# Optimization experiments

Hardware: AMD Instinct MI355X
Metric: run time of the kernel (lower is better)

## Reference

```python
import jax, jax.numpy as jnp
import numpy as np

B, C, H, W = 4, 512, 48, 48
DQ = C // 8  # inter_rate = 8
N = H * W
EPS = 1e-5


def _local_mask(radius):
    r = np.arange(N) // W
    c = np.arange(N) % W
    d = np.maximum(np.abs(r[:, None] - r[None, :]), np.abs(c[:, None] - c[None, :]))
    return jnp.asarray(d <= radius)


def setup_inputs() -> dict:
    key = jax.random.key(0)
    ks = jax.random.split(key, 12)
    def nrm(k, shape, scale=0.04):
        return jax.random.normal(k, shape, dtype=jnp.float32) * scale
    zc = jnp.zeros((C,), jnp.float32)
    oc = jnp.ones((C,), jnp.float32)
    return {
        "x": jax.random.normal(ks[0], (B, C, H, W), dtype=jnp.float32),
        "Wq": nrm(ks[1], (DQ, C)), "bq": jnp.zeros((DQ,), jnp.float32),
        "Wk": nrm(ks[2], (DQ, C)), "bk": jnp.zeros((DQ,), jnp.float32),
        "Wv": nrm(ks[3], (C, C)), "bv": zc,
        "conv1_w": nrm(ks[4], (C, C, 3, 3)),
        "bn1_w": oc, "bn1_b": zc, "bn1_m": zc, "bn1_v": oc,
        "conv2_w": nrm(ks[5], (C, C, 3, 3)),
        "bn2_w": oc, "bn2_b": zc, "bn2_m": zc, "bn2_v": oc,
        "sig1_w": nrm(ks[6], (C, C)), "sig1_b": zc,
        "sig2_w": nrm(ks[7], (C, C)), "sig2_b": zc,
        "gamma": jnp.full((1,), 0.5, jnp.float32),
        "gamma1": jnp.full((1,), 0.3, jnp.float32),
        "gamma2": jnp.full((1,), 0.2, jnp.float32),
        "mask1": _local_mask(6),
        "mask2": _local_mask(12),
    }


def _masked_softmax(e, mask):
    # exp(e)*mask / sum(exp(e)*mask) == softmax with -inf outside mask
    e = e - jnp.max(e, axis=-1, keepdims=True)
    w = jnp.exp(e) * mask.astype(e.dtype)
    return w / jnp.sum(w, axis=-1, keepdims=True)


def _conv1x1(t, w, b):
    return jnp.einsum('bchw,dc->bdhw', t, w) + b[None, :, None, None]


def _conv3x3_bn_relu(t, w, g, beta, mu, var):
    y = jax.lax.conv_general_dilated(t, w, (1, 1), 'SAME',
                                     dimension_numbers=('NCHW', 'OIHW', 'NCHW'))
    scale = (g / jnp.sqrt(var + EPS))[None, :, None, None]
    y = (y - mu[None, :, None, None]) * scale + beta[None, :, None, None]
    return jax.nn.relu(y)


def _forward(x, Wq, bq, Wk, bk, Wv, bv, conv1_w, bn1_w, bn1_b, bn1_m, bn1_v,
             conv2_w, bn2_w, bn2_b, bn2_m, bn2_v, sig1_w, sig1_b, sig2_w, sig2_b,
             gamma, gamma1, gamma2, mask1, mask2):
    b, c, h, w = x.shape
    n = h * w
    q = _conv1x1(x, Wq, bq).reshape(b, -1, n)   # [B, d, N]
    k = _conv1x1(x, Wk, bk).reshape(b, -1, n)   # [B, d, N]
    energy = jnp.einsum('bdn,bdm->bnm', q, k)   # [B, N, N] (query rows)
    a0 = jax.nn.softmax(energy, axis=-1)
    a1 = _masked_softmax(energy, mask1)
    a2 = _masked_softmax(energy, mask2)
    v = _conv1x1(x, Wv, bv).reshape(b, c, n)
    # torch: bmm(value, attention.permute(0,2,1)) -> out[b,c,m] = sum_n v[b,c,n]*a[m,n]
    out0 = jnp.einsum('bcn,bmn->bcm', v, a0).reshape(b, c, h, w)
    out0 = gamma * out0 + x
    out0 = _conv3x3_bn_relu(out0, conv1_w, bn1_w, bn1_b, bn1_m, bn1_v)
    s1 = (jax.nn.sigmoid(_conv1x1(out0, sig1_w, sig1_b)) * out0).reshape(b, c, n)
    out1 = jnp.einsum('bcn,bmn->bcm', s1, a1).reshape(b, c, h, w)
    out1 = gamma1 * out1 + out0
    out1 = _conv3x3_bn_relu(out1, conv2_w, bn2_w, bn2_b, bn2_m, bn2_v)
    s2 = (jax.nn.sigmoid(_conv1x1(out1, sig2_w, sig2_b)) * out1).reshape(b, c, n)
    out2 = jnp.einsum('bcn,bmn->bcm', s2, a2).reshape(b, c, h, w)
    return gamma2 * out2 + out1


def reference(x, Wq, bq, Wk, bk, Wv, bv, conv1_w, bn1_w, bn1_b, bn1_m, bn1_v,
              conv2_w, bn2_w, bn2_b, bn2_m, bn2_v, sig1_w, sig1_b, sig2_w, sig2_b,
              gamma, gamma1, gamma2, mask1, mask2):
    return _forward(x, Wq, bq, Wk, bk, Wv, bv, conv1_w, bn1_w, bn1_b, bn1_m, bn1_v,
                    conv2_w, bn2_w, bn2_b, bn2_m, bn2_v, sig1_w, sig1_b, sig2_w, sig2_b,
                    gamma, gamma1, gamma2, mask1, mask2)
```

## Files before the change

kernel.cpp:

```cpp
#include <hip/hip_runtime.h>
#include <math.h>

#define BB 4
#define CC 512
#define HH 48
#define WW 48
#define NN 2304
#define DDQ 64
#define LDSP 72
#define PW 50
#define PROWS 2500

typedef __attribute__((ext_vector_type(4))) float f32x4;
typedef __attribute__((ext_vector_type(8))) _Float16 half8;
typedef __attribute__((ext_vector_type(4))) _Float16 half4;

__device__ __forceinline__ int imax(int a, int b) { return a > b ? a : b; }
__device__ __forceinline__ int imin(int a, int b) { return a < b ? a : b; }
__device__ __forceinline__ int prow(int m) {
    int h = m / WW, w = m - h * WW;
    return (h + 1) * PW + (w + 1);
}

typedef __attribute__((address_space(1))) unsigned int g_u32;
typedef __attribute__((address_space(3))) unsigned int l_u32;
__device__ __forceinline__ void gl16(const _Float16* g, _Float16* l) {
    __builtin_amdgcn_global_load_lds((g_u32*)g, (l_u32*)l, 16, 0, 0);
}

#define BWAVE_IDX()                                  \
    int tid = threadIdx.x;                           \
    int wave = tid >> 6, lane = tid & 63;            \
    int wm = (wave >> 1) * 64, wn = (wave & 1) * 32; \
    int x = lane & 15, qq = lane >> 4;

__device__ __forceinline__ half8 fragld(const _Float16* T, int r, int c) {
    int kb = c ^ (r & 7);
    return *(const half8*)(T + r * 64 + kb * 8);
}

__device__ __forceinline__ void btile(const _Float16* As, const _Float16* Bs,
                                      f32x4 acc[4][2], int wm, int wn, int x, int qq) {
#pragma unroll
    for (int ks = 0; ks < 2; ++ks) {
        int c = ks * 4 + qq;
        half8 a0 = fragld(As, wm + x, c);
        half8 a1 = fragld(As, wm + 16 + x, c);
        half8 a2 = fragld(As, wm + 32 + x, c);
        half8 a3 = fragld(As, wm + 48 + x, c);
        half8 b0 = fragld(Bs, wn + x, c);
        half8 b1 = fragld(Bs, wn + 16 + x, c);
        acc[0][0] = __builtin_amdgcn_mfma_f32_16x16x32_f16(a0, b0, acc[0][0], 0, 0, 0);
        acc[0][1] = __builtin_amdgcn_mfma_f32_16x16x32_f16(a0, b1, acc[0][1], 0, 0, 0);
        acc[1][0] = __builtin_amdgcn_mfma_f32_16x16x32_f16(a1, b0, acc[1][0], 0, 0, 0);
        acc[1][1] = __builtin_amdgcn_mfma_f32_16x16x32_f16(a1, b1, acc[1][1], 0, 0, 0);
        acc[2][0] = __builtin_amdgcn_mfma_f32_16x16x32_f16(a2, b0, acc[2][0], 0, 0, 0);
        acc[2][1] = __builtin_amdgcn_mfma_f32_16x16x32_f16(a2, b1, acc[2][1], 0, 0, 0);
        acc[3][0] = __builtin_amdgcn_mfma_f32_16x16x32_f16(a3, b0, acc[3][0], 0, 0, 0);
        acc[3][1] = __builtin_amdgcn_mfma_f32_16x16x32_f16(a3, b1, acc[3][1], 0, 0, 0);
    }
}

#define BACC_INIT()                                         \
    f32x4 zf = {0.f, 0.f, 0.f, 0.f};                        \
    f32x4 acc[4][2];                                        \
    _Pragma("unroll") for (int i_ = 0; i_ < 4; ++i_) {      \
        acc[i_][0] = zf; acc[i_][1] = zf; }

#define SLOT_A(i) int sb = (wave * 4 + (i)) * 64; int s = sb + lane; \
                  int r = s >> 3, kb = s & 7; int koff = ((kb ^ (r & 7)) << 3);
#define SLOT_B(i) int sb = (wave * 2 + (i)) * 64; int s = sb + lane; \
                  int r = s >> 3, kb = s & 7; int koff = ((kb ^ (r & 7)) << 3);

__device__ __forceinline__ void stage_rows(_Float16* dst, const _Float16* __restrict__ src,
                                           int ld, int row0, int k0, int tid) {
#pragma unroll
    for (int i = 0; i < 2; ++i) {
        int s = tid * 2 + i;
        int r = s >> 3, off = (s & 7) << 3;
        *(half8*)(dst + r * LDSP + off) =
            *(const half8*)(src + (size_t)(row0 + r) * ld + k0 + off);
    }
}
__device__ __forceinline__ void mfma_tile(const _Float16* As, const _Float16* Bs,
                                          f32x4 acc[2][2], int wm, int wn, int x, int qq) {
#pragma unroll
    for (int ks = 0; ks < 2; ++ks) {
        int kof = ks * 32 + qq * 8;
        half8 a0 = *(const half8*)(As + (wm + x) * LDSP + kof);
        half8 a1 = *(const half8*)(As + (wm + 16 + x) * LDSP + kof);
        half8 b0 = *(const half8*)(Bs + (wn + x) * LDSP + kof);
        half8 b1 = *(const half8*)(Bs + (wn + 16 + x) * LDSP + kof);
        acc[0][0] = __builtin_amdgcn_mfma_f32_16x16x32_f16(a0, b0, acc[0][0], 0, 0, 0);
        acc[0][1] = __builtin_amdgcn_mfma_f32_16x16x32_f16(a0, b1, acc[0][1], 0, 0, 0);
        acc[1][0] = __builtin_amdgcn_mfma_f32_16x16x32_f16(a1, b0, acc[1][0], 0, 0, 0);
        acc[1][1] = __builtin_amdgcn_mfma_f32_16x16x32_f16(a1, b1, acc[1][1], 0, 0, 0);
    }
}
#define WAVE_IDX()                             \
    int tid = threadIdx.x;                     \
    int wave = tid >> 6, lane = tid & 63;      \
    int wm = (wave >> 1) * 32, wn = (wave & 1) * 32; \
    int x = lane & 15, qq = lane >> 4;
#define ACC_INIT()                             \
    f32x4 zf = {0.f, 0.f, 0.f, 0.f};           \
    f32x4 acc[2][2];                           \
    acc[0][0] = zf; acc[0][1] = zf; acc[1][0] = zf; acc[1][1] = zf;

__global__ __launch_bounds__(256) void k_f32_to_f16(const float* __restrict__ src,
                                                    _Float16* __restrict__ dst, int n) {
    for (int i = blockIdx.x * 256 + threadIdx.x; i < n; i += gridDim.x * 256)
        dst[i] = (_Float16)src[i];
}

__global__ __launch_bounds__(256) void k_repack_conv(const float* __restrict__ w,
                                                     _Float16* __restrict__ dst) {
    int i = blockIdx.x * 256 + threadIdx.x;
    if (i >= 9 * CC * CC) return;
    int r = i / (CC * CC);
    int rem = i - r * CC * CC;
    int co = rem / CC, ci = rem - (rem / CC) * CC;
    dst[i] = (_Float16)w[((size_t)co * CC + ci) * 9 + r];
}

__global__ __launch_bounds__(256) void k_transpose_x(const float* __restrict__ x,
                                                     _Float16* __restrict__ xT) {
    __shared__ float tile[32][33];
    int b = blockIdx.z;
    int c0 = blockIdx.y * 32, n0 = blockIdx.x * 32;
    int tx = threadIdx.x & 31, ty = threadIdx.x >> 5;
    const float* xb = x + (size_t)b * CC * NN;
#pragma unroll
    for (int rr = 0; rr < 32; rr += 8)
        tile[ty + rr][tx] = xb[(size_t)(c0 + ty + rr) * NN + n0 + tx];
    __syncthreads();
    _Float16* xTb = xT + (size_t)b * NN * CC;
#pragma unroll
    for (int rr = 0; rr < 32; rr += 8)
        xTb[(size_t)(n0 + ty + rr) * CC + c0 + tx] = (_Float16)tile[tx][ty + rr];
}

__global__ __launch_bounds__(256) void k_qkproj(const _Float16* __restrict__ Wq,
                                                const _Float16* __restrict__ Wk,
                                                const float* __restrict__ bq,
                                                const float* __restrict__ bk,
                                                const _Float16* __restrict__ xT,
                                                _Float16* __restrict__ qT,
                                                _Float16* __restrict__ kT) {
    __shared__ _Float16 As[64 * LDSP];
    __shared__ _Float16 Bs[64 * LDSP];
    WAVE_IDX();
    int j0 = blockIdx.x * 64, b = blockIdx.z;
    const _Float16* Wp = blockIdx.y ? Wk : Wq;
    const float* bias = blockIdx.y ? bk : bq;
    _Float16* outT = blockIdx.y ? kT : qT;
    const _Float16* xTb = xT + (size_t)b * NN * CC;
    ACC_INIT();
    for (int kc = 0; kc < CC; kc += 64) {
        stage_rows(As, Wp, CC, 0, kc, tid);
        stage_rows(Bs, xTb, CC, j0, kc, tid);
        __syncthreads();
        mfma_tile(As, Bs, acc, wm, wn, x, qq);
        __syncthreads();
    }
#pragma unroll
    for (int ms = 0; ms < 2; ++ms) {
        int R0 = wm + ms * 16 + qq * 4;
#pragma unroll
        for (int ns = 0; ns < 2; ++ns) {
            int Ccol = j0 + wn + ns * 16 + x;
            half4 t;
            t.x = (_Float16)(acc[ms][ns][0] + bias[R0 + 0]);
            t.y = (_Float16)(acc[ms][ns][1] + bias[R0 + 1]);
            t.z = (_Float16)(acc[ms][ns][2] + bias[R0 + 2]);
            t.w = (_Float16)(acc[ms][ns][3] + bias[R0 + 3]);
            *(half4*)(outT + ((size_t)b * NN + Ccol) * DDQ + R0) = t;
        }
    }
}

template <int EPI, int PAD>
__global__ __launch_bounds__(256) void k_cgemm(const _Float16* __restrict__ W,
                                               const float* __restrict__ bias,
                                               const _Float16* __restrict__ Bsrc,
                                               const float* __restrict__ gate,
                                               _Float16* __restrict__ out) {
    __shared__ _Float16 As[128 * 64];
    __shared__ _Float16 Bs[64 * 64];
    BWAVE_IDX();
    int j0 = blockIdx.x * 64, i0 = blockIdx.y * 128, b = blockIdx.z;
    const _Float16* Bb = Bsrc + (size_t)b * (PAD ? (size_t)PROWS * CC : (size_t)NN * CC);

    const _Float16* aSrc[4]; int aOf[4];
#pragma unroll
    for (int i = 0; i < 4; ++i) {
        SLOT_A(i);
        aSrc[i] = W + (size_t)(i0 + r) * CC + koff;
        aOf[i] = sb * 8;
    }
    const _Float16* bSrc[2]; int bOf[2];
#pragma unroll
    for (int i = 0; i < 2; ++i) {
        SLOT_B(i);
        int row = PAD ? prow(j0 + r) : (j0 + r);
        bSrc[i] = Bb + (size_t)row * CC + koff;
        bOf[i] = sb * 8;
    }
    BACC_INIT();
    for (int kc = 0; kc < CC; kc += 64) {
        __syncthreads();
#pragma unroll
        for (int i = 0; i < 4; ++i) gl16(aSrc[i] + kc, As + aOf[i]);
#pragma unroll
        for (int i = 0; i < 2; ++i) gl16(bSrc[i] + kc, Bs + bOf[i]);
        __syncthreads();
        btile(As, Bs, acc, wm, wn, x, qq);
    }
#pragma unroll
    for (int mt = 0; mt < 4; ++mt) {
        int R0 = i0 + wm + mt * 16 + qq * 4;
#pragma unroll
        for (int nt = 0; nt < 2; ++nt) {
            int Ccol = j0 + wn + nt * 16 + x;
#pragma unroll
            for (int e = 0; e < 4; ++e) {
                float v = acc[mt][nt][e] + bias[R0 + e];
                size_t idx = ((size_t)b * CC + R0 + e) * NN + Ccol;
                if (EPI == 1) v = gate[idx] / (1.f + __expf(-v));
                out[idx] = (_Float16)v;
            }
        }
    }
}

__global__ __launch_bounds__(256) void k_energy(const _Float16* __restrict__ qT,
                                                const _Float16* __restrict__ kT,
                                                float* __restrict__ E, int rad) {
    __shared__ _Float16 As[64 * LDSP];
    __shared__ _Float16 Bs[64 * LDSP];
    WAVE_IDX();
    int j0 = blockIdx.x * 64, i0 = blockIdx.y * 64, b = blockIdx.z;
    if (rad > 0) {
        int hlo = i0 / WW, hhi = (i0 + 63) / WW;
        int h2lo = imax(0, hlo - rad), h2hi = imin(HH - 1, hhi + rad);
        int nlo = (h2lo * WW) & ~63;
        int nhi = imin(NN, ((h2hi + 1) * WW + 63) & ~63);
        if (j0 + 64 <= nlo || j0 >= nhi) return;
    }
    ACC_INIT();
    stage_rows(As, qT + (size_t)b * NN * DDQ, DDQ, i0, 0, tid);
    stage_rows(Bs, kT + (size_t)b * NN * DDQ, DDQ, j0, 0, tid);
    __syncthreads();
    mfma_tile(As, Bs, acc, wm, wn, x, qq);
#pragma unroll
    for (int ms = 0; ms < 2; ++ms) {
        int R0 = i0 + wm + ms * 16 + qq * 4;
#pragma unroll
        for (int ns = 0; ns < 2; ++ns) {
            int Ccol = j0 + wn + ns * 16 + x;
#pragma unroll
            for (int e = 0; e < 4; ++e)
                E[((size_t)b * NN + R0 + e) * NN + Ccol] = acc[ms][ns][e];
        }
    }
}

__global__ __launch_bounds__(256) void k_softmax(float* __restrict__ E, int rad) {
    __shared__ float red[256];
    int tid = threadIdx.x;
    int m = blockIdx.x, b = blockIdx.y;
    float* e = E + ((size_t)b * NN + m) * NN;
    _Float16* a = (_Float16*)e;
    int own_lo = 0, own_hi = NN, nlo = 0, nhi = NN;
    int mcol = m % WW;
    if (rad > 0) {
        int hm = m / WW;
        int oh_lo = imax(0, hm - rad), oh_hi = imin(HH - 1, hm + rad);
        own_lo = oh_lo * WW; own_hi = (oh_hi + 1) * WW;
        int i0 = m & ~63;
        int hlo = i0 / WW, hhi = (i0 + 63) / WW;
        int h2lo = imax(0, hlo - rad), h2hi = imin(HH - 1, hhi + rad);
        nlo = (h2lo * WW) & ~63;
        nhi = imin(NN, ((h2hi + 1) * WW + 63) & ~63);
    }
    int v0 = own_lo >> 2, v1 = own_hi >> 2;

    float mx = -1e30f;
    for (int n4 = v0 + tid; n4 < v1; n4 += 256) {
        float4 v = *(const float4*)(e + n4 * 4);
        mx = fmaxf(fmaxf(fmaxf(mx, v.x), v.y), fmaxf(v.z, v.w));
    }
    red[tid] = mx; __syncthreads();
    for (int s = 128; s > 0; s >>= 1) {
        if (tid < s) red[tid] = fmaxf(red[tid], red[tid + s]);
        __syncthreads();
    }
    mx = red[0]; __syncthreads();

    f32x4 wloc[3];
    float ls = 0.f;
#pragma unroll
    for (int ii = 0; ii < 3; ++ii) {
        int n4 = v0 + tid + ii * 256;
        if (n4 < v1) {
            float4 v = *(const float4*)(e + n4 * 4);
            f32x4 w;
            w[0] = __expf(v.x - mx); w[1] = __expf(v.y - mx);
            w[2] = __expf(v.z - mx); w[3] = __expf(v.w - mx);
            if (rad > 0) {
                int cb = (n4 * 4) % WW;
#pragma unroll
                for (int j = 0; j < 4; ++j) {
                    int dc = mcol - (cb + j); if (dc < 0) dc = -dc;
                    if (dc > rad) w[j] = 0.f;
                }
            }
            wloc[ii] = w;
            ls += w[0] + w[1] + w[2] + w[3];
        }
    }
    red[tid] = ls; __syncthreads();
    for (int s = 128; s > 0; s >>= 1) {
        if (tid < s) red[tid] += red[tid + s];
        __syncthreads();
    }
    float inv = 1.f / red[0];
#pragma unroll
    for (int ii = 0; ii < 3; ++ii) {
        int n4 = v0 + tid + ii * 256;
        if (n4 < v1) {
            half4 h;
            h.x = (_Float16)(wloc[ii][0] * inv);
            h.y = (_Float16)(wloc[ii][1] * inv);
            h.z = (_Float16)(wloc[ii][2] * inv);
            h.w = (_Float16)(wloc[ii][3] * inv);
            *(half4*)(a + n4 * 4) = h;
        }
    }
    for (int n = nlo + tid; n < own_lo; n += 256) a[n] = (_Float16)0.f;
    for (int n = own_hi + tid; n < nhi; n += 256) a[n] = (_Float16)0.f;
}

__global__ __launch_bounds__(256) void k_attn(const _Float16* __restrict__ A,
                                              const _Float16* __restrict__ attn,
                                              const float* __restrict__ res,
                                              const float* __restrict__ gamma,
                                              float* __restrict__ outF,
                                              _Float16* __restrict__ outT, int rad) {
    __shared__ _Float16 As[128 * 64];
    __shared__ _Float16 Bs[64 * 64];
    BWAVE_IDX();
    int j0 = blockIdx.x * 64, i0 = blockIdx.y * 128, b = blockIdx.z;
    int klo = 0, khi = NN;
    if (rad > 0) {
        int hlo = j0 / WW, hhi = (j0 + 63) / WW;
        int h2lo = imax(0, hlo - rad), h2hi = imin(HH - 1, hhi + rad);
        klo = (h2lo * WW) & ~63;
        khi = imin(NN, ((h2hi + 1) * WW + 63) & ~63);
    }
    const _Float16* Ab = A + (size_t)b * CC * NN;
    const _Float16* Tb = attn + (size_t)b * NN * (2 * NN);

    const _Float16* aSrc[4]; int aOf[4];
#pragma unroll
    for (int i = 0; i < 4; ++i) {
        SLOT_A(i);
        aSrc[i] = Ab + (size_t)(i0 + r) * NN + koff;
        aOf[i] = sb * 8;
    }
    const _Float16* bSrc[2]; int bOf[2];
#pragma unroll
    for (int i = 0; i < 2; ++i) {
        SLOT_B(i);
        bSrc[i] = Tb + (size_t)(j0 + r) * (2 * NN) + koff;
        bOf[i] = sb * 8;
    }
    BACC_INIT();
    for (int kc = klo; kc < khi; kc += 64) {
        __syncthreads();
#pragma unroll
        for (int i = 0; i < 4; ++i) gl16(aSrc[i] + kc, As + aOf[i]);
#pragma unroll
        for (int i = 0; i < 2; ++i) gl16(bSrc[i] + kc, Bs + bOf[i]);
        __syncthreads();
        btile(As, Bs, acc, wm, wn, x, qq);
    }
    float g = gamma[0];
#pragma unroll
    for (int mt = 0; mt < 4; ++mt) {
        int R0 = i0 + wm + mt * 16 + qq * 4;
#pragma unroll
        for (int nt = 0; nt < 2; ++nt) {
            int Ccol = j0 + wn + nt * 16 + x;
            float v[4];
#pragma unroll
            for (int e = 0; e < 4; ++e)
                v[e] = g * acc[mt][nt][e] + res[((size_t)b * CC + R0 + e) * NN + Ccol];
            if (outT) {
                half4 t;
                t.x = (_Float16)v[0]; t.y = (_Float16)v[1];
                t.z = (_Float16)v[2]; t.w = (_Float16)v[3];
                *(half4*)(outT + ((size_t)b * PROWS + prow(Ccol)) * CC + R0) = t;
            }
            if (outF) {
#pragma unroll
                for (int e = 0; e < 4; ++e)
                    outF[((size_t)b * CC + R0 + e) * NN + Ccol] = v[e];
            }
        }
    }
}

__global__ __launch_bounds__(256) void k_conv3(const _Float16* __restrict__ Arep,
                                               const _Float16* __restrict__ Tpad,
                                               const float* __restrict__ bng,
                                               const float* __restrict__ bnb,
                                               const float* __restrict__ bnm,
                                               const float* __restrict__ bnv,
                                               float* __restrict__ outF,
                                               _Float16* __restrict__ outT) {
    __shared__ _Float16 As[128 * 64];
    __shared__ _Float16 Bs[64 * 64];
    BWAVE_IDX();
    int j0 = blockIdx.x * 64, i0 = blockIdx.y * 128, b = blockIdx.z;
    const _Float16* Tb = Tpad + (size_t)b * PROWS * CC;

    size_t aRow[4]; int aOf[4];
#pragma unroll
    for (int i = 0; i < 4; ++i) {
        SLOT_A(i);
        aRow[i] = (size_t)(i0 + r) * CC + koff;
        aOf[i] = sb * 8;
    }
    int bPr[2], bKoff[2], bOf[2];
#pragma unroll
    for (int i = 0; i < 2; ++i) {
        SLOT_B(i);
        bPr[i] = prow(j0 + r);
        bKoff[i] = koff;
        bOf[i] = sb * 8;
    }
    BACC_INIT();
#pragma unroll
    for (int rt = 0; rt < 9; ++rt) {
        int dh = rt / 3 - 1, dw = rt - (rt / 3) * 3 - 1;
        int shift = dh * PW + dw;
        const _Float16* Ar = Arep + (size_t)rt * CC * CC;
        for (int ci0 = 0; ci0 < CC; ci0 += 64) {
            __syncthreads();
#pragma unroll
            for (int i = 0; i < 4; ++i) gl16(Ar + aRow[i] + ci0, As + aOf[i]);
#pragma unroll
            for (int i = 0; i < 2; ++i)
                gl16(Tb + (size_t)(bPr[i] + shift) * CC + ci0 + bKoff[i], Bs + bOf[i]);
            __syncthreads();
            btile(As, Bs, acc, wm, wn, x, qq);
        }
    }
#pragma unroll
    for (int mt = 0; mt < 4; ++mt) {
        int R0 = i0 + wm + mt * 16 + qq * 4;
        float sc[4], sh[4];
#pragma unroll
        for (int e = 0; e < 4; ++e) {
            sc[e] = bng[R0 + e] * rsqrtf(bnv[R0 + e] + 1e-5f);
            sh[e] = bnb[R0 + e] - bnm[R0 + e] * sc[e];
        }
#pragma unroll
        for (int nt = 0; nt < 2; ++nt) {
            int Ccol = j0 + wn + nt * 16 + x;
            float v[4];
#pragma unroll
            for (int e = 0; e < 4; ++e) {
                float t = acc[mt][nt][e] * sc[e] + sh[e];
                v[e] = t > 0.f ? t : 0.f;
                outF[((size_t)b * CC + R0 + e) * NN + Ccol] = v[e];
            }
            half4 t4;
            t4.x = (_Float16)v[0]; t4.y = (_Float16)v[1];
            t4.z = (_Float16)v[2]; t4.w = (_Float16)v[3];
            *(half4*)(outT + ((size_t)b * PROWS + prow(Ccol)) * CC + R0) = t4;
        }
    }
}

extern "C" void kernel_launch(void* const* d_in, const int* in_sizes, int n_in,
                              void* d_out, int out_size, void* d_ws, size_t ws_size,
                              hipStream_t stream) {
    const float* xin  = (const float*)d_in[0];
    const float* Wq   = (const float*)d_in[1];
    const float* bq   = (const float*)d_in[2];
    const float* Wk   = (const float*)d_in[3];
    const float* bk   = (const float*)d_in[4];
    const float* Wv   = (const float*)d_in[5];
    const float* bv   = (const float*)d_in[6];
    const float* c1w  = (const float*)d_in[7];
    const float* bn1w = (const float*)d_in[8];
    const float* bn1b = (const float*)d_in[9];
    const float* bn1m = (const float*)d_in[10];
    const float* bn1v = (const float*)d_in[11];
    const float* c2w  = (const float*)d_in[12];
    const float* bn2w = (const float*)d_in[13];
    const float* bn2b = (const float*)d_in[14];
    const float* bn2m = (const float*)d_in[15];
    const float* bn2v = (const float*)d_in[16];
    const float* s1w  = (const float*)d_in[17];
    const float* s1b  = (const float*)d_in[18];
    const float* s2w  = (const float*)d_in[19];
    const float* s2b  = (const float*)d_in[20];
    const float* gamma  = (const float*)d_in[21];
    const float* gamma1 = (const float*)d_in[22];
    const float* gamma2 = (const float*)d_in[23];

    float* out = (float*)d_out;

    char* p = (char*)d_ws;
    float*    E     = (float*)p;    p += (size_t)BB * NN * NN * 4;
    _Float16* xT    = (_Float16*)p; p += (size_t)BB * NN * CC * 2;
    _Float16* qT    = (_Float16*)p; p += (size_t)BB * NN * DDQ * 2;
    _Float16* kT    = (_Float16*)p; p += (size_t)BB * NN * DDQ * 2;
    _Float16* vsB   = (_Float16*)p; p += (size_t)BB * CC * NN * 2;
    _Float16* TattnP= (_Float16*)p; p += (size_t)BB * PROWS * CC * 2;
    _Float16* TconvP= (_Float16*)p; p += (size_t)BB * PROWS * CC * 2;
    float*    rR    = (float*)p;    p += (size_t)BB * CC * NN * 4;
    _Float16* wq_h  = (_Float16*)p; p += (size_t)DDQ * CC * 2;
    _Float16* wk_h  = (_Float16*)p; p += (size_t)DDQ * CC * 2;
    _Float16* wv_h  = (_Float16*)p; p += (size_t)CC * CC * 2;
    _Float16* s1_h  = (_Float16*)p; p += (size_t)CC * CC * 2;
    _Float16* s2_h  = (_Float16*)p; p += (size_t)CC * CC * 2;
    _Float16* crep1 = (_Float16*)p; p += (size_t)9 * CC * CC * 2;
    _Float16* crep2 = (_Float16*)p; p += (size_t)9 * CC * CC * 2;

    dim3 blk(256);

    hipMemsetAsync(TattnP, 0, (size_t)BB * PROWS * CC * 2, stream);
    hipMemsetAsync(TconvP, 0, (size_t)BB * PROWS * CC * 2, stream);

    k_f32_to_f16<<<dim3(128), blk, 0, stream>>>(Wq, wq_h, DDQ * CC);
    k_f32_to_f16<<<dim3(128), blk, 0, stream>>>(Wk, wk_h, DDQ * CC);
    k_f32_to_f16<<<dim3(1024), blk, 0, stream>>>(Wv, wv_h, CC * CC);
    k_f32_to_f16<<<dim3(1024), blk, 0, stream>>>(s1w, s1_h, CC * CC);
    k_f32_to_f16<<<dim3(1024), blk, 0, stream>>>(s2w, s2_h, CC * CC);
    k_repack_conv<<<dim3((9 * CC * CC + 255) / 256), blk, 0, stream>>>(c1w, crep1);
    k_repack_conv<<<dim3((9 * CC * CC + 255) / 256), blk, 0, stream>>>(c2w, crep2);
    k_transpose_x<<<dim3(NN / 32, CC / 32, BB), blk, 0, stream>>>(xin, xT);

    dim3 gQK(NN / 64, 2, BB);
    dim3 gE (NN / 64, NN / 64, BB);
    dim3 gSm(NN, BB);
    dim3 gBig(NN / 64, CC / 128, BB);

    const _Float16* attnH = (const _Float16*)E;

    k_qkproj<<<gQK, blk, 0, stream>>>(wq_h, wk_h, bq, bk, xT, qT, kT);
    k_cgemm<0, 0><<<gBig, blk, 0, stream>>>(wv_h, bv, xT, nullptr, vsB);

    k_energy<<<gE, blk, 0, stream>>>(qT, kT, E, -1);
    k_softmax<<<gSm, blk, 0, stream>>>(E, -1);
    k_attn<<<gBig, blk, 0, stream>>>(vsB, attnH, xin, gamma, nullptr, TattnP, -1);
    k_conv3<<<gBig, blk, 0, stream>>>(crep1, TattnP, bn1w, bn1b, bn1m, bn1v, rR, TconvP);

    k_cgemm<1, 1><<<gBig, blk, 0, stream>>>(s1_h, s1b, TconvP, rR, vsB);
    k_energy<<<gE, blk, 0, stream>>>(qT, kT, E, 6);
    k_softmax<<<gSm, blk, 0, stream>>>(E, 6);
    k_attn<<<gBig, blk, 0, stream>>>(vsB, attnH, rR, gamma1, nullptr, TattnP, 6);
    k_conv3<<<gBig, blk, 0, stream>>>(crep2, TattnP, bn2w, bn2b, bn2m, bn2v, rR, TconvP);

    k_cgemm<1, 1><<<gBig, blk, 0, stream>>>(s2_h, s2b, TconvP, rR, vsB);
    k_energy<<<gE, blk, 0, stream>>>(qT, kT, E, 12);
    k_softmax<<<gSm, blk, 0, stream>>>(E, 12);
    k_attn<<<gBig, blk, 0, stream>>>(vsB, attnH, rR, gamma2, out, nullptr, 12);
}
```

Measured before the change: 557.1 us.

## Fuse energy GEMM and masked softmax into one two-pass kernel writing fp16 attention

Replaces the separate energy kernel, which wrote a full fp32 N×N matrix, and the row-softmax kernel with one kernel per 64-row query block. The fused kernel computes QK^T twice: the first pass accumulates row sums of exp and the second writes normalized fp16 probabilities straight to a compact attention buffer. The locality mask is applied per element inside the kernel. The max subtraction is dropped, which depends on energies being small enough for exp not to overflow. Weight-cast and conv-repack launches are also merged into fewer multi-tensor launches. This removes fp32 energy traffic in exchange for recomputing the GEMM and running a smaller grid.

```diff
diff --git a/kernel.cpp b/kernel.cpp
--- a/kernel.cpp
+++ b/kernel.cpp
@@ -107,14 +107,24 @@
     f32x4 acc[2][2];                           \
     acc[0][0] = zf; acc[0][1] = zf; acc[1][0] = zf; acc[1][1] = zf;
 
-__global__ __launch_bounds__(256) void k_f32_to_f16(const float* __restrict__ src,
-                                                    _Float16* __restrict__ dst, int n) {
+__global__ __launch_bounds__(256) void k_cast_multi(const float* __restrict__ s0,
+                                                    const float* __restrict__ s1,
+                                                    const float* __restrict__ s2,
+                                                    _Float16* __restrict__ d0,
+                                                    _Float16* __restrict__ d1,
+                                                    _Float16* __restrict__ d2, int n) {
+    const float* s = blockIdx.y == 0 ? s0 : (blockIdx.y == 1 ? s1 : s2);
+    _Float16* d = blockIdx.y == 0 ? d0 : (blockIdx.y == 1 ? d1 : d2);
     for (int i = blockIdx.x * 256 + threadIdx.x; i < n; i += gridDim.x * 256)
-        dst[i] = (_Float16)src[i];
-}
-
-__global__ __launch_bounds__(256) void k_repack_conv(const float* __restrict__ w,
-                                                     _Float16* __restrict__ dst) {
+        d[i] = (_Float16)s[i];
+}
+
+__global__ __launch_bounds__(256) void k_repack_conv2(const float* __restrict__ w1,
+                                                      const float* __restrict__ w2,
+                                                      _Float16* __restrict__ d1,
+                                                      _Float16* __restrict__ d2) {
+    const float* w = blockIdx.y ? w2 : w1;
+    _Float16* dst = blockIdx.y ? d2 : d1;
     int i = blockIdx.x * 256 + threadIdx.x;
     if (i >= 9 * CC * CC) return;
     int r = i / (CC * CC);
@@ -233,112 +243,117 @@
     }
 }
 
-__global__ __launch_bounds__(256) void k_energy(const _Float16* __restrict__ qT,
-                                                const _Float16* __restrict__ kT,
-                                                float* __restrict__ E, int rad) {
-    __shared__ _Float16 As[64 * LDSP];
-    __shared__ _Float16 Bs[64 * LDSP];
+__global__ __launch_bounds__(256) void k_fused_sm(const _Float16* __restrict__ qT,
+                                                  const _Float16* __restrict__ kT,
+                                                  _Float16* __restrict__ attn, int rad) {
+    __shared__ _Float16 qs[64 * LDSP];
+    __shared__ _Float16 ks[64 * LDSP];
+    __shared__ float Ef[64][68];
+    __shared__ _Float16 Eh[64 * 72];
+    __shared__ float psum[256];
+    __shared__ float linvS[64];
     WAVE_IDX();
-    int j0 = blockIdx.x * 64, i0 = blockIdx.y * 64, b = blockIdx.z;
+    int i0 = blockIdx.x * 64, b = blockIdx.y;
+
+    int klo = 0, khi = NN;
     if (rad > 0) {
         int hlo = i0 / WW, hhi = (i0 + 63) / WW;
         int h2lo = imax(0, hlo - rad), h2hi = imin(HH - 1, hhi + rad);
-        int nlo = (h2lo * WW) & ~63;
-        int nhi = imin(NN, ((h2hi + 1) * WW + 63) & ~63);
-        if (j0 + 64 <= nlo || j0 >= nhi) return;
-    }
-    ACC_INIT();
-    stage_rows(As, qT + (size_t)b * NN * DDQ, DDQ, i0, 0, tid);
-    stage_rows(Bs, kT + (size_t)b * NN * DDQ, DDQ, j0, 0, tid);
-    __syncthreads();
-    mfma_tile(As, Bs, acc, wm, wn, x, qq);
-#pragma unroll
-    for (int ms = 0; ms < 2; ++ms) {
-        int R0 = i0 + wm + ms * 16 + qq * 4;
+        klo = (h2lo * WW) & ~63;
+        khi = imin(NN, ((h2hi + 1) * WW + 63) & ~63);
+    }
+
+    int hm8[8], cm8[8];
+#pragma unroll
+    for (int ms = 0; ms < 2; ++ms)
+#pragma unroll
+        for (int e = 0; e < 4; ++e) {
+            int gm = i0 + wm + ms * 16 + qq * 4 + e;
+            hm8[ms * 4 + e] = gm / WW;
+            cm8[ms * 4 + e] = gm % WW;
+        }
+
+    stage_rows(qs, qT + (size_t)b * NN * DDQ, DDQ, i0, 0, tid);
+
+    float l_i = 0.f;
+    const _Float16* kTb = kT + (size_t)b * NN * DDQ;
+
+    for (int j0 = klo; j0 < khi; j0 += 64) {
+        __syncthreads();
+        stage_rows(ks, kTb, DDQ, j0, 0, tid);
+        __syncthreads();
+        ACC_INIT();
+        mfma_tile(qs, ks, acc, wm, wn, x, qq);
 #pragma unroll
         for (int ns = 0; ns < 2; ++ns) {
-            int Ccol = j0 + wn + ns * 16 + x;
-#pragma unroll
-            for (int e = 0; e < 4; ++e)
-                E[((size_t)b * NN + R0 + e) * NN + Ccol] = acc[ms][ns][e];
-        }
-    }
-}
-
-__global__ __launch_bounds__(256) void k_softmax(float* __restrict__ E, int rad) {
-    __shared__ float red[256];
-    int tid = threadIdx.x;
-    int m = blockIdx.x, b = blockIdx.y;
-    float* e = E + ((size_t)b * NN + m) * NN;
-    _Float16* a = (_Float16*)e;
-    int own_lo = 0, own_hi = NN, nlo = 0, nhi = NN;
-    int mcol = m % WW;
-    if (rad > 0) {
-        int hm = m / WW;
-        int oh_lo = imax(0, hm - rad), oh_hi = imin(HH - 1, hm + rad);
-        own_lo = oh_lo * WW; own_hi = (oh_hi + 1) * WW;
-        int i0 = m & ~63;
-        int hlo = i0 / WW, hhi = (i0 + 63) / WW;
-        int h2lo = imax(0, hlo - rad), h2hi = imin(HH - 1, hhi + rad);
-        nlo = (h2lo * WW) & ~63;
-        nhi = imin(NN, ((h2hi + 1) * WW + 63) & ~63);
-    }
-    int v0 = own_lo >> 2, v1 = own_hi >> 2;
-
-    float mx = -1e30f;
-    for (int n4 = v0 + tid; n4 < v1; n4 += 256) {
-        float4 v = *(const float4*)(e + n4 * 4);
-        mx = fmaxf(fmaxf(fmaxf(mx, v.x), v.y), fmaxf(v.z, v.w));
-    }
-    red[tid] = mx; __syncthreads();
-    for (int s = 128; s > 0; s >>= 1) {
-        if (tid < s) red[tid] = fmaxf(red[tid], red[tid + s]);
-        __syncthreads();
-    }
-    mx = red[0]; __syncthreads();
-
-    f32x4 wloc[3];
-    float ls = 0.f;
-#pragma unroll
-    for (int ii = 0; ii < 3; ++ii) {
-        int n4 = v0 + tid + ii * 256;
-        if (n4 < v1) {
-            float4 v = *(const float4*)(e + n4 * 4);
-            f32x4 w;
-            w[0] = __expf(v.x - mx); w[1] = __expf(v.y - mx);
-            w[2] = __expf(v.z - mx); w[3] = __expf(v.w - mx);
-            if (rad > 0) {
-                int cb = (n4 * 4) % WW;
-#pragma unroll
-                for (int j = 0; j < 4; ++j) {
-                    int dc = mcol - (cb + j); if (dc < 0) dc = -dc;
-                    if (dc > rad) w[j] = 0.f;
+            int col = wn + ns * 16 + x;
+            int gn = j0 + col;
+            int hn = gn / WW, cn = gn % WW;
+#pragma unroll
+            for (int ms = 0; ms < 2; ++ms)
+#pragma unroll
+                for (int e = 0; e < 4; ++e) {
+                    int ri = ms * 4 + e;
+                    bool valid = true;
+                    if (rad > 0) {
+                        int dh = hm8[ri] - hn; if (dh < 0) dh = -dh;
+                        int dc = cm8[ri] - cn; if (dc < 0) dc = -dc;
+                        valid = (dh <= rad) && (dc <= rad);
+                    }
+                    Ef[wm + ms * 16 + qq * 4 + e][col] =
+                        valid ? __expf(acc[ms][ns][e]) : 0.f;
                 }
-            }
-            wloc[ii] = w;
-            ls += w[0] + w[1] + w[2] + w[3];
-        }
-    }
-    red[tid] = ls; __syncthreads();
-    for (int s = 128; s > 0; s >>= 1) {
-        if (tid < s) red[tid] += red[tid + s];
-        __syncthreads();
-    }
-    float inv = 1.f / red[0];
-#pragma unroll
-    for (int ii = 0; ii < 3; ++ii) {
-        int n4 = v0 + tid + ii * 256;
-        if (n4 < v1) {
-            half4 h;
-            h.x = (_Float16)(wloc[ii][0] * inv);
-            h.y = (_Float16)(wloc[ii][1] * inv);
-            h.z = (_Float16)(wloc[ii][2] * inv);
-            h.w = (_Float16)(wloc[ii][3] * inv);
-            *(half4*)(a + n4 * 4) = h;
-        }
-    }
-    for (int n = nlo + tid; n < own_lo; n += 256) a[n] = (_Float16)0.f;
-    for (int n = own_hi + tid; n < nhi; n += 256) a[n] = (_Float16)0.f;
+        }
+        __syncthreads();
+        {
+            int r = tid >> 2, qtr = tid & 3;
+            float s = 0.f;
+#pragma unroll
+            for (int j = 0; j < 16; ++j) s += Ef[r][qtr * 16 + j];
+            psum[tid] = s;
+        }
+        __syncthreads();
+        if (tid < 64)
+            l_i += psum[tid * 4] + psum[tid * 4 + 1] + psum[tid * 4 + 2] + psum[tid * 4 + 3];
+    }
+    if (tid < 64) linvS[tid] = 1.f / fmaxf(l_i, 1e-30f);
+
+    for (int j0 = klo; j0 < khi; j0 += 64) {
+        __syncthreads();
+        stage_rows(ks, kTb, DDQ, j0, 0, tid);
+        __syncthreads();
+        ACC_INIT();
+        mfma_tile(qs, ks, acc, wm, wn, x, qq);
+#pragma unroll
+        for (int ns = 0; ns < 2; ++ns) {
+            int col = wn + ns * 16 + x;
+            int gn = j0 + col;
+            int hn = gn / WW, cn = gn % WW;
+#pragma unroll
+            for (int ms = 0; ms < 2; ++ms)
+#pragma unroll
+                for (int e = 0; e < 4; ++e) {
+                    int ri = ms * 4 + e;
+                    int row = wm + ms * 16 + qq * 4 + e;
+                    bool valid = true;
+                    if (rad > 0) {
+                        int dh = hm8[ri] - hn; if (dh < 0) dh = -dh;
+                        int dc = cm8[ri] - cn; if (dc < 0) dc = -dc;
+                        valid = (dh <= rad) && (dc <= rad);
+                    }
+                    float w = valid ? __expf(acc[ms][ns][e]) * linvS[row] : 0.f;
+                    Eh[row * 72 + col] = (_Float16)w;
+                }
+        }
+        __syncthreads();
+#pragma unroll
+        for (int t = 0; t < 2; ++t) {
+            int s = tid + t * 256;
+            int r = s >> 3, cg = (s & 7) << 3;
+            *(half8*)(attn + ((size_t)b * NN + i0 + r) * NN + j0 + cg) =
+                *(const half8*)(Eh + r * 72 + cg);
+        }
+    }
 }
 
 __global__ __launch_bounds__(256) void k_attn(const _Float16* __restrict__ A,
@@ -359,7 +374,7 @@
         khi = imin(NN, ((h2hi + 1) * WW + 63) & ~63);
     }
     const _Float16* Ab = A + (size_t)b * CC * NN;
-    const _Float16* Tb = attn + (size_t)b * NN * (2 * NN);
+    const _Float16* Tb = attn + (size_t)b * NN * NN;
 
     const _Float16* aSrc[4]; int aOf[4];
 #pragma unroll
@@ -372,7 +387,7 @@
 #pragma unroll
     for (int i = 0; i < 2; ++i) {
         SLOT_B(i);
-        bSrc[i] = Tb + (size_t)(j0 + r) * (2 * NN) + koff;
+        bSrc[i] = Tb + (size_t)(j0 + r) * NN + koff;
         bOf[i] = sb * 8;
     }
     BACC_INIT();
@@ -515,7 +530,7 @@
     float* out = (float*)d_out;
 
     char* p = (char*)d_ws;
-    float*    E     = (float*)p;    p += (size_t)BB * NN * NN * 4;
+    _Float16* attn  = (_Float16*)p; p += (size_t)BB * NN * NN * 2;
     _Float16* xT    = (_Float16*)p; p += (size_t)BB * NN * CC * 2;
     _Float16* qT    = (_Float16*)p; p += (size_t)BB * NN * DDQ * 2;
     _Float16* kT    = (_Float16*)p; p += (size_t)BB * NN * DDQ * 2;
@@ -536,38 +551,28 @@
     hipMemsetAsync(TattnP, 0, (size_t)BB * PROWS * CC * 2, stream);
     hipMemsetAsync(TconvP, 0, (size_t)BB * PROWS * CC * 2, stream);
 
-    k_f32_to_f16<<<dim3(128), blk, 0, stream>>>(Wq, wq_h, DDQ * CC);
-    k_f32_to_f16<<<dim3(128), blk, 0, stream>>>(Wk, wk_h, DDQ * CC);
-    k_f32_to_f16<<<dim3(1024), blk, 0, stream>>>(Wv, wv_h, CC * CC);
-    k_f32_to_f16<<<dim3(1024), blk, 0, stream>>>(s1w, s1_h, CC * CC);
-    k_f32_to_f16<<<dim3(1024), blk, 0, stream>>>(s2w, s2_h, CC * CC);
-    k_repack_conv<<<dim3((9 * CC * CC + 255) / 256), blk, 0, stream>>>(c1w, crep1);
-    k_repack_conv<<<dim3((9 * CC * CC + 255) / 256), blk, 0, stream>>>(c2w, crep2);
+    k_cast_multi<<<dim3(128, 2), blk, 0, stream>>>(Wq, Wk, nullptr, wq_h, wk_h, nullptr, DDQ * CC);
+    k_cast_multi<<<dim3(1024, 3), blk, 0, stream>>>(Wv, s1w, s2w, wv_h, s1_h, s2_h, CC * CC);
+    k_repack_conv2<<<dim3((9 * CC * CC + 255) / 256, 2), blk, 0, stream>>>(c1w, c2w, crep1, crep2);
     k_transpose_x<<<dim3(NN / 32, CC / 32, BB), blk, 0, stream>>>(xin, xT);
 
     dim3 gQK(NN / 64, 2, BB);
-    dim3 gE (NN / 64, NN / 64, BB);
-    dim3 gSm(NN, BB);
+    dim3 gSm(NN / 64, BB);
     dim3 gBig(NN / 64, CC / 128, BB);
-
-    const _Float16* attnH = (const _Float16*)E;
 
     k_qkproj<<<gQK, blk, 0, stream>>>(wq_h, wk_h, bq, bk, xT, qT, kT);
     k_cgemm<0, 0><<<gBig, blk, 0, stream>>>(wv_h, bv, xT, nullptr, vsB);
 
-    k_energy<<<gE, blk, 0, stream>>>(qT, kT, E, -1);
-    k_softmax<<<gSm, blk, 0, stream>>>(E, -1);
-    k_attn<<<gBig, blk, 0, stream>>>(vsB, attnH, xin, gamma, nullptr, TattnP, -1);
+    k_fused_sm<<<gSm, blk, 0, stream>>>(qT, kT, attn, -1);
+    k_attn<<<gBig, blk, 0, stream>>>(vsB, attn, xin, gamma, nullptr, TattnP, -1);
     k_conv3<<<gBig, blk, 0, stream>>>(crep1, TattnP, bn1w, bn1b, bn1m, bn1v, rR, TconvP);
 
     k_cgemm<1, 1><<<gBig, blk, 0, stream>>>(s1_h, s1b, TconvP, rR, vsB);
-    k_energy<<<gE, blk, 0, stream>>>(qT, kT, E, 6);
-    k_softmax<<<gSm, blk, 0, stream>>>(E, 6);
-    k_attn<<<gBig, blk, 0, stream>>>(vsB, attnH, rR, gamma1, nullptr, TattnP, 6);
+    k_fused_sm<<<gSm, blk, 0, stream>>>(qT, kT, attn, 6);
+    k_attn<<<gBig, blk, 0, stream>>>(vsB, attn, rR, gamma1, nullptr, TattnP, 6);
     k_conv3<<<gBig, blk, 0, stream>>>(crep2, TattnP, bn2w, bn2b, bn2m, bn2v, rR, TconvP);
 
     k_cgemm<1, 1><<<gBig, blk, 0, stream>>>(s2_h, s2b, TconvP, rR, vsB);
-    k_energy<<<gE, blk, 0, stream>>>(qT, kT, E, 12);
-    k_softmax<<<gSm, blk, 0, stream>>>(E, 12);
-    k_attn<<<gBig, blk, 0, stream>>>(vsB, attnH, rR, gamma2, out, nullptr, 12);
-}
+    k_fused_sm<<<gSm, blk, 0, stream>>>(qT, kT, attn, 12);
+    k_attn<<<gBig, blk, 0, stream>>>(vsB, attn, rR, gamma2, out, nullptr, 12);
+}
```

New measurement: 673.2 us. 1.21x slower.
